# Optimization experiments

Measured on AMD Instinct MI355X. Metric: run time of the kernel, lower is better.

The kernel has to match this reference:

```python
import jax, jax.numpy as jnp
import numpy as np

D_HEAD = 64
SCALE = D_HEAD ** 0.5
MASK_FILL = -10000.0


def setup_inputs() -> dict:
    key = jax.random.key(0)
    kq, kk, kv, km = jax.random.split(key, 4)
    B, H, S, D = 2, 16, 2048, D_HEAD
    query = jax.random.normal(kq, (B, H, S, D), dtype=jnp.float32)
    k = jax.random.normal(kk, (B, H, S, D), dtype=jnp.float32)
    v = jax.random.normal(kv, (B, H, S, D), dtype=jnp.float32)
    attn_mask = jax.random.randint(km, (B, H, S, S), 0, 2).astype(jnp.bool_)
    return {"query": query, "key": k, "value": v, "attn_mask": attn_mask}


def reference(query, key, value, attn_mask):
    # scores: [B, H, Sq, Sk]
    scores = jnp.einsum("bhqd,bhkd->bhqk", query, key) / SCALE
    scores = jnp.where(attn_mask, MASK_FILL, scores)
    attn_prob = jax.nn.softmax(scores, axis=-1)
    context = jnp.einsum("bhqk,bhkd->bhqd", attn_prob, value)
    return (context, attn_prob)
```

## Files before the change

### kernel.cpp

```cpp
#include <hip/hip_runtime.h>
#include <cstdint>
#include <cstddef>

#define S_LEN 2048
#define D_HEAD 64
#define NBH 32

typedef __attribute__((ext_vector_type(8))) short short8;
typedef __attribute__((ext_vector_type(8))) unsigned short ushort8;
typedef __attribute__((ext_vector_type(4))) unsigned short us4;
typedef __attribute__((ext_vector_type(4))) unsigned int ui4;
typedef __attribute__((ext_vector_type(4))) float floatx4;

__device__ __forceinline__ unsigned short f2bf(float f){
  union { float f; unsigned int i; } v; v.f = f;
  unsigned int u = v.i;
  u += 0x7fffu + ((u >> 16) & 1u);
  return (unsigned short)(u >> 16);
}
__device__ __forceinline__ float bf2f(unsigned short u){
  union { unsigned int i; float f; } v; v.i = ((unsigned int)u) << 16; return v.f;
}

__device__ __forceinline__ int swz(int row, int col){
  return row * S_LEN + ((((col >> 3) ^ row) & 15) << 3)
                     + (((col >> 3) & ~15) << 3) + (col & 7);
}

__global__ void detect_mask_kernel(const unsigned int* __restrict__ m, int* __restrict__ flag){
  __shared__ int f;
  if (threadIdx.x == 0) f = 0;
  __syncthreads();
  if (m[threadIdx.x] > 1u) atomicOr(&f, 1);
  __syncthreads();
  if (threadIdx.x == 0) *flag = f;
}

__global__ void packmask_kernel(const void* __restrict__ maskp, const int* __restrict__ flag,
                                unsigned int* __restrict__ pm){
  const int w = blockIdx.x * 256 + threadIdx.x;
  unsigned int bits = 0;
  if (*flag){
    const unsigned char* mb = (const unsigned char*)maskp + (size_t)w * 32;
    const ui4 x0 = *(const ui4*)(mb);
    const ui4 x1 = *(const ui4*)(mb + 16);
#pragma unroll
    for (int i = 0; i < 4; ++i){
      const unsigned int a = x0[i], b = x1[i];
#pragma unroll
      for (int j = 0; j < 4; ++j){
        bits |= (((a >> (8 * j)) & 0xffu) ? 1u : 0u) << (4 * i + j);
        bits |= (((b >> (8 * j)) & 0xffu) ? 1u : 0u) << (16 + 4 * i + j);
      }
    }
  } else {
    const unsigned int* mi = (const unsigned int*)maskp + (size_t)w * 32;
#pragma unroll
    for (int i = 0; i < 8; ++i){
      const ui4 x = *(const ui4*)(mi + i * 4);
#pragma unroll
      for (int j = 0; j < 4; ++j)
        bits |= (x[j] ? 1u : 0u) << (i * 4 + j);
    }
  }
  pm[w] = bits;
}

__global__ void convK_kernel(const float* __restrict__ K, unsigned short* __restrict__ Kb){
  const size_t i = ((size_t)blockIdx.x * 256 + threadIdx.x) * 8;
  floatx4 x0 = *(const floatx4*)(K + i);
  floatx4 x1 = *(const floatx4*)(K + i + 4);
  ushort8 o;
#pragma unroll
  for (int j = 0; j < 4; ++j){ o[j] = f2bf(x0[j]); o[4 + j] = f2bf(x1[j]); }
  *(ushort8*)(Kb + i) = o;
}

__global__ void vtrans_kernel(const float* __restrict__ V, unsigned short* __restrict__ Vt){
  const int bh = blockIdx.y;
  const int n  = threadIdx.x & 63;
  const int k0 = blockIdx.x * 32 + (threadIdx.x >> 6) * 8;
  const float* Vp = V + (size_t)bh * S_LEN * D_HEAD;
  ushort8 o;
#pragma unroll
  for (int i = 0; i < 8; ++i) o[i] = f2bf(Vp[(size_t)(k0 + i) * D_HEAD + n]);
  *(ushort8*)(Vt + (size_t)bh * D_HEAD * S_LEN + (size_t)n * S_LEN + k0) = o;
}

__global__ __launch_bounds__(256, 2) void attn_kernel(
    const float* __restrict__ Q, const unsigned short* __restrict__ Kb,
    const unsigned int* __restrict__ pm,
    const unsigned short* __restrict__ Vt,
    float* __restrict__ prob, float* __restrict__ ctx,
    float* __restrict__ redg, float* __restrict__ invg){

  __shared__ unsigned short Pt[16 * S_LEN];

  const int lin  = blockIdx.y * gridDim.x + blockIdx.x;
  const int xcd  = lin & 7;
  const int sub  = lin >> 3;
  const int bh   = xcd * 4 + (sub & 3);
  const int qt   = sub >> 2;

  const int q0g  = bh * S_LEN + qt * 16;
  const int tid  = threadIdx.x;
  const int wave = tid >> 6;
  const int lane = tid & 63;
  const int quad = lane >> 4;
  const int r16  = lane & 15;
  const int blk  = bh * gridDim.x + qt;

  const float* qrow = Q + (size_t)(q0g + r16) * D_HEAD + quad * 8;
  short8 a0, a1;
  {
    floatx4 x0 = *(const floatx4*)(qrow);
    floatx4 x1 = *(const floatx4*)(qrow + 4);
    floatx4 y0 = *(const floatx4*)(qrow + 32);
    floatx4 y1 = *(const floatx4*)(qrow + 36);
#pragma unroll
    for (int j = 0; j < 4; ++j){
      a0[j] = (short)f2bf(x0[j]); a0[4 + j] = (short)f2bf(x1[j]);
      a1[j] = (short)f2bf(y0[j]); a1[4 + j] = (short)f2bf(y1[j]);
    }
  }

  const unsigned int* mrow = pm + (size_t)(q0g + r16) * 64 + wave * 16;
  const unsigned short* kbase = Kb + (size_t)bh * S_LEN * D_HEAD;

  float racc = 0.f;
  ui4 mcur = *(const ui4*)(mrow);
  for (int tt = 0; tt < 4; ++tt){
    const ui4 mnext = (tt < 3) ? *(const ui4*)(mrow + (tt + 1) * 4) : mcur;
#pragma unroll
    for (int tj = 0; tj < 8; ++tj){
      const int t  = tt * 8 + tj;
      const int s0 = wave * 512 + t * 16;
      const unsigned short* krow = kbase + (size_t)(s0 + r16) * D_HEAD + quad * 8;
      const short8 b0 = *(const short8*)(krow);
      const short8 b1 = *(const short8*)(krow + 32);
      floatx4 c = {0.f, 0.f, 0.f, 0.f};
      c = __builtin_amdgcn_mfma_f32_16x16x32_bf16(b0, a0, c, 0, 0, 0);
      c = __builtin_amdgcn_mfma_f32_16x16x32_bf16(b1, a1, c, 0, 0, 0);
      const unsigned int bits = mcur[tj >> 1] >> (16 * (tj & 1) + 4 * quad);
      us4 w;
#pragma unroll
      for (int i = 0; i < 4; ++i){
        const float p = ((bits >> i) & 1u) ? 0.0f : __expf(c[i] * 0.125f);
        racc += p;
        w[i] = f2bf(p);
      }
      *(us4*)(&Pt[swz(r16, s0 + quad * 4)]) = w;
    }
    mcur = mnext;
  }

  racc += __shfl_xor(racc, 16);
  racc += __shfl_xor(racc, 32);
  if (lane < 16) redg[(size_t)blk * 64 + wave * 16 + lane] = racc;
  __syncthreads();
  if (tid < 16){
    float s = 0.f;
#pragma unroll
    for (int w = 0; w < 4; ++w) s += redg[(size_t)blk * 64 + w * 16 + tid];
    invg[(size_t)blk * 16 + tid] = (s > 0.f) ? (1.0f / s) : 0.0f;
  }
  __syncthreads();

  float inv4[4];
#pragma unroll
  for (int i = 0; i < 4; ++i) inv4[i] = invg[(size_t)blk * 16 + quad * 4 + i];

  const unsigned short* vrow = Vt + (size_t)bh * D_HEAD * S_LEN
                                  + (size_t)(wave * 16 + r16) * S_LEN + quad * 8;
  floatx4 cA = {0.f,0.f,0.f,0.f}, cB = {0.f,0.f,0.f,0.f};
#pragma unroll 8
  for (int kk = 0; kk < 64; kk += 2){
    const short8 bv0 = *(const short8*)(vrow + kk * 32);
    const short8 aa0 = *(const short8*)(&Pt[swz(r16, kk * 32 + quad * 8)]);
    const short8 bv1 = *(const short8*)(vrow + (kk + 1) * 32);
    const short8 aa1 = *(const short8*)(&Pt[swz(r16, (kk + 1) * 32 + quad * 8)]);
    cA = __builtin_amdgcn_mfma_f32_16x16x32_bf16(aa0, bv0, cA, 0, 0, 0);
    cB = __builtin_amdgcn_mfma_f32_16x16x32_bf16(aa1, bv1, cB, 0, 0, 0);
  }
#pragma unroll
  for (int i = 0; i < 4; ++i)
    ctx[(size_t)(q0g + quad * 4 + i) * D_HEAD + wave * 16 + r16] = (cA[i] + cB[i]) * inv4[i];

#pragma unroll
  for (int rr = 0; rr < 4; ++rr){
    const int row = wave * 4 + rr;
    const float iv = invg[(size_t)blk * 16 + row];
    float* pg = prob + (size_t)(q0g + row) * S_LEN;
#pragma unroll
    for (int j = 0; j < 4; ++j){
      const int col = j * 512 + lane * 8;
      const ushort8 u = *(const ushort8*)(&Pt[swz(row, col)]);
      floatx4 o0, o1;
#pragma unroll
      for (int e = 0; e < 4; ++e){
        o0[e] = bf2f(u[e]) * iv;
        o1[e] = bf2f(u[4 + e]) * iv;
      }
      *(floatx4*)(pg + col)     = o0;
      *(floatx4*)(pg + col + 4) = o1;
    }
  }
}

extern "C" void kernel_launch(void* const* d_in, const int* in_sizes, int n_in,
                              void* d_out, int out_size, void* d_ws, size_t ws_size,
                              hipStream_t stream) {
  const float* Q = (const float*)d_in[0];
  const float* K = (const float*)d_in[1];
  const float* V = (const float*)d_in[2];
  const void*  M = d_in[3];

  float* ctx  = (float*)d_out;
  float* prob = (float*)d_out + (size_t)NBH * S_LEN * D_HEAD;

  unsigned int* pm = (unsigned int*)d_out;

  int*   flag = (int*)d_ws;
  float* redg = (float*)((char*)d_ws + (1u << 12));
  float* invg = (float*)((char*)d_ws + (1u << 12) + (1u << 20));
  unsigned short* Kb = (unsigned short*)((char*)d_ws + (2u << 20));
  unsigned short* Vt = (unsigned short*)((char*)d_ws + (10u << 20));

  hipLaunchKernelGGL(detect_mask_kernel, dim3(1), dim3(256), 0, stream,
                     (const unsigned int*)M, flag);
  hipLaunchKernelGGL(packmask_kernel, dim3((NBH * S_LEN * S_LEN / 32) / 256), dim3(256),
                     0, stream, M, flag, pm);
  hipLaunchKernelGGL(convK_kernel, dim3(2048), dim3(256), 0, stream, K, Kb);
  hipLaunchKernelGGL(vtrans_kernel, dim3(S_LEN/32, NBH), dim3(256), 0, stream, V, Vt);
  hipLaunchKernelGGL(attn_kernel, dim3(S_LEN/16, NBH), dim3(256), 0, stream,
                     Q, Kb, pm, Vt, prob, ctx, redg, invg);
}
```

Before: 1.148 ms.

## Fuse probability writeback into PV loop and keep row-sum reduction in LDS

Moves the per-row sum reduction from global workspace into shared memory, which removes one barrier and the global round trip. Writes the normalized probabilities inside the PV MFMA loop from the already-loaded P fragments, with each wave handling one quarter of the columns, instead of running a separate LDS re-read pass. Also uses exp2 with a prescaled constant, packed bf16 conversion via inline asm, and nontemporal loads and stores for the mask and outputs. The prob stores now interleave with the MFMA loop in a branch tied to the wave, which may affect scheduling, and the packed conversion may round differently from the manual rounding.

```diff
diff --git a/kernel.cpp b/kernel.cpp
--- a/kernel.cpp
+++ b/kernel.cpp
@@ -8,7 +8,7 @@
 
 typedef __attribute__((ext_vector_type(8))) short short8;
 typedef __attribute__((ext_vector_type(8))) unsigned short ushort8;
-typedef __attribute__((ext_vector_type(4))) unsigned short us4;
+typedef __attribute__((ext_vector_type(2))) unsigned int ui2;
 typedef __attribute__((ext_vector_type(4))) unsigned int ui4;
 typedef __attribute__((ext_vector_type(4))) float floatx4;
 
@@ -20,6 +20,11 @@
 }
 __device__ __forceinline__ float bf2f(unsigned short u){
   union { unsigned int i; float f; } v; v.i = ((unsigned int)u) << 16; return v.f;
+}
+__device__ __forceinline__ unsigned int cvtpk(float lo, float hi){
+  unsigned int r;
+  asm("v_cvt_pk_bf16_f32 %0, %1, %2" : "=v"(r) : "v"(lo), "v"(hi));
+  return r;
 }
 
 __device__ __forceinline__ int swz(int row, int col){
@@ -41,9 +46,9 @@
   const int w = blockIdx.x * 256 + threadIdx.x;
   unsigned int bits = 0;
   if (*flag){
-    const unsigned char* mb = (const unsigned char*)maskp + (size_t)w * 32;
-    const ui4 x0 = *(const ui4*)(mb);
-    const ui4 x1 = *(const ui4*)(mb + 16);
+    const ui4* mb = (const ui4*)((const unsigned char*)maskp + (size_t)w * 32);
+    const ui4 x0 = __builtin_nontemporal_load(mb);
+    const ui4 x1 = __builtin_nontemporal_load(mb + 1);
 #pragma unroll
     for (int i = 0; i < 4; ++i){
       const unsigned int a = x0[i], b = x1[i];
@@ -54,10 +59,10 @@
       }
     }
   } else {
-    const unsigned int* mi = (const unsigned int*)maskp + (size_t)w * 32;
+    const ui4* mi = (const ui4*)((const unsigned int*)maskp + (size_t)w * 32);
 #pragma unroll
     for (int i = 0; i < 8; ++i){
-      const ui4 x = *(const ui4*)(mi + i * 4);
+      const ui4 x = __builtin_nontemporal_load(mi + i);
 #pragma unroll
       for (int j = 0; j < 4; ++j)
         bits |= (x[j] ? 1u : 0u) << (i * 4 + j);
@@ -91,10 +96,10 @@
     const float* __restrict__ Q, const unsigned short* __restrict__ Kb,
     const unsigned int* __restrict__ pm,
     const unsigned short* __restrict__ Vt,
-    float* __restrict__ prob, float* __restrict__ ctx,
-    float* __restrict__ redg, float* __restrict__ invg){
+    float* __restrict__ prob, float* __restrict__ ctx){
 
   __shared__ unsigned short Pt[16 * S_LEN];
+  __shared__ float redL[64];
 
   const int lin  = blockIdx.y * gridDim.x + blockIdx.x;
   const int xcd  = lin & 7;
@@ -108,7 +113,6 @@
   const int lane = tid & 63;
   const int quad = lane >> 4;
   const int r16  = lane & 15;
-  const int blk  = bh * gridDim.x + qt;
 
   const float* qrow = Q + (size_t)(q0g + r16) * D_HEAD + quad * 8;
   short8 a0, a1;
@@ -142,68 +146,68 @@
       c = __builtin_amdgcn_mfma_f32_16x16x32_bf16(b0, a0, c, 0, 0, 0);
       c = __builtin_amdgcn_mfma_f32_16x16x32_bf16(b1, a1, c, 0, 0, 0);
       const unsigned int bits = mcur[tj >> 1] >> (16 * (tj & 1) + 4 * quad);
-      us4 w;
+      float p[4];
 #pragma unroll
       for (int i = 0; i < 4; ++i){
-        const float p = ((bits >> i) & 1u) ? 0.0f : __expf(c[i] * 0.125f);
-        racc += p;
-        w[i] = f2bf(p);
+        p[i] = ((bits >> i) & 1u) ? 0.0f
+             : __builtin_amdgcn_exp2f(c[i] * 0.18033688011f);
+        racc += p[i];
       }
-      *(us4*)(&Pt[swz(r16, s0 + quad * 4)]) = w;
+      const ui2 w = { cvtpk(p[0], p[1]), cvtpk(p[2], p[3]) };
+      *(ui2*)(&Pt[swz(r16, s0 + quad * 4)]) = w;
     }
     mcur = mnext;
   }
 
   racc += __shfl_xor(racc, 16);
   racc += __shfl_xor(racc, 32);
-  if (lane < 16) redg[(size_t)blk * 64 + wave * 16 + lane] = racc;
+  if (lane < 16) redL[wave * 16 + lane] = racc;
   __syncthreads();
-  if (tid < 16){
-    float s = 0.f;
-#pragma unroll
-    for (int w = 0; w < 4; ++w) s += redg[(size_t)blk * 64 + w * 16 + tid];
-    invg[(size_t)blk * 16 + tid] = (s > 0.f) ? (1.0f / s) : 0.0f;
-  }
-  __syncthreads();
-
-  float inv4[4];
-#pragma unroll
-  for (int i = 0; i < 4; ++i) inv4[i] = invg[(size_t)blk * 16 + quad * 4 + i];
+  const float s = redL[r16] + redL[16 + r16] + redL[32 + r16] + redL[48 + r16];
+  const float inv_r = (s > 0.f) ? (1.0f / s) : 0.0f;
 
   const unsigned short* vrow = Vt + (size_t)bh * D_HEAD * S_LEN
                                   + (size_t)(wave * 16 + r16) * S_LEN + quad * 8;
+  float* prow = prob + (size_t)(q0g + r16) * S_LEN;
   floatx4 cA = {0.f,0.f,0.f,0.f}, cB = {0.f,0.f,0.f,0.f};
-#pragma unroll 8
-  for (int kk = 0; kk < 64; kk += 2){
-    const short8 bv0 = *(const short8*)(vrow + kk * 32);
-    const short8 aa0 = *(const short8*)(&Pt[swz(r16, kk * 32 + quad * 8)]);
-    const short8 bv1 = *(const short8*)(vrow + (kk + 1) * 32);
-    const short8 aa1 = *(const short8*)(&Pt[swz(r16, (kk + 1) * 32 + quad * 8)]);
-    cA = __builtin_amdgcn_mfma_f32_16x16x32_bf16(aa0, bv0, cA, 0, 0, 0);
-    cB = __builtin_amdgcn_mfma_f32_16x16x32_bf16(aa1, bv1, cB, 0, 0, 0);
-  }
-#pragma unroll
-  for (int i = 0; i < 4; ++i)
-    ctx[(size_t)(q0g + quad * 4 + i) * D_HEAD + wave * 16 + r16] = (cA[i] + cB[i]) * inv4[i];
-
-#pragma unroll
-  for (int rr = 0; rr < 4; ++rr){
-    const int row = wave * 4 + rr;
-    const float iv = invg[(size_t)blk * 16 + row];
-    float* pg = prob + (size_t)(q0g + row) * S_LEN;
-#pragma unroll
-    for (int j = 0; j < 4; ++j){
-      const int col = j * 512 + lane * 8;
-      const ushort8 u = *(const ushort8*)(&Pt[swz(row, col)]);
-      floatx4 o0, o1;
-#pragma unroll
-      for (int e = 0; e < 4; ++e){
-        o0[e] = bf2f(u[e]) * iv;
-        o1[e] = bf2f(u[4 + e]) * iv;
+
+  for (int g = 0; g < 4; ++g){
+    const bool wr = (g == wave);
+#pragma unroll 4
+    for (int k2 = 0; k2 < 16; k2 += 2){
+      const int kk = g * 16 + k2;
+      const short8 bv0 = *(const short8*)(vrow + kk * 32);
+      const short8 aa0 = *(const short8*)(&Pt[swz(r16, kk * 32 + quad * 8)]);
+      const short8 bv1 = *(const short8*)(vrow + (kk + 1) * 32);
+      const short8 aa1 = *(const short8*)(&Pt[swz(r16, (kk + 1) * 32 + quad * 8)]);
+      cA = __builtin_amdgcn_mfma_f32_16x16x32_bf16(aa0, bv0, cA, 0, 0, 0);
+      cB = __builtin_amdgcn_mfma_f32_16x16x32_bf16(aa1, bv1, cB, 0, 0, 0);
+      if (wr){
+        floatx4 o0, o1, o2, o3;
+#pragma unroll
+        for (int e = 0; e < 4; ++e){
+          o0[e] = bf2f((unsigned short)aa0[e])     * inv_r;
+          o1[e] = bf2f((unsigned short)aa0[4 + e]) * inv_r;
+          o2[e] = bf2f((unsigned short)aa1[e])     * inv_r;
+          o3[e] = bf2f((unsigned short)aa1[4 + e]) * inv_r;
+        }
+        float* pg = prow + kk * 32 + quad * 8;
+        __builtin_nontemporal_store(o0, (floatx4*)(pg));
+        __builtin_nontemporal_store(o1, (floatx4*)(pg + 4));
+        __builtin_nontemporal_store(o2, (floatx4*)(pg + 32));
+        __builtin_nontemporal_store(o3, (floatx4*)(pg + 36));
       }
-      *(floatx4*)(pg + col)     = o0;
-      *(floatx4*)(pg + col + 4) = o1;
-    }
+    }
+  }
+
+  float inv4[4];
+#pragma unroll
+  for (int i = 0; i < 4; ++i) inv4[i] = __shfl(inv_r, quad * 4 + i, 64);
+#pragma unroll
+  for (int i = 0; i < 4; ++i){
+    const float v = (cA[i] + cB[i]) * inv4[i];
+    __builtin_nontemporal_store(v,
+        ctx + (size_t)(q0g + quad * 4 + i) * D_HEAD + wave * 16 + r16);
   }
 }
 
@@ -221,8 +225,6 @@
   unsigned int* pm = (unsigned int*)d_out;
 
   int*   flag = (int*)d_ws;
-  float* redg = (float*)((char*)d_ws + (1u << 12));
-  float* invg = (float*)((char*)d_ws + (1u << 12) + (1u << 20));
   unsigned short* Kb = (unsigned short*)((char*)d_ws + (2u << 20));
   unsigned short* Vt = (unsigned short*)((char*)d_ws + (10u << 20));
 
@@ -233,5 +235,5 @@
   hipLaunchKernelGGL(convK_kernel, dim3(2048), dim3(256), 0, stream, K, Kb);
   hipLaunchKernelGGL(vtrans_kernel, dim3(S_LEN/32, NBH), dim3(256), 0, stream, V, Vt);
   hipLaunchKernelGGL(attn_kernel, dim3(S_LEN/16, NBH), dim3(256), 0, stream,
-                     Q, Kb, pm, Vt, prob, ctx, redg, invg);
-}
+                     Q, Kb, pm, Vt, prob, ctx);
+}
```

Result: slower. 1.209 ms (+5.3%).
